# Kernel optimization log

Hardware: AMD Instinct MI355X
Metric: run time of the kernel (lower is better)

The kernel has to match this reference:

```python
import jax, jax.numpy as jnp
import numpy as np

N = 100000   # nodes
E = 1600000  # edges (before self loops)
F = 64       # num_features
H = 64       # hidden_channels
C = 10       # num_classes
G = 128      # graphs in batch
NEG_SLOPE = 0.2


def setup_inputs() -> dict:
    key = jax.random.key(0)
    ks = jax.random.split(key, 16)
    x = jax.random.normal(ks[0], (N, F), dtype=jnp.float32)
    edge_index = jax.random.randint(ks[1], (2, E), 0, N, dtype=jnp.int64)
    batch = jnp.sort(jax.random.randint(ks[2], (N,), 0, G, dtype=jnp.int64))
    def glorot(k, shape):
        fan = shape[0] + shape[-1]
        return jax.random.uniform(k, shape, jnp.float32, -1.0, 1.0) * np.sqrt(6.0 / fan)
    return {
        "x": x, "edge_index": edge_index, "batch": batch,
        # GATConv 1 (F -> H)
        "W1": glorot(ks[3], (F, H)), "as1": glorot(ks[4], (H,)), "ad1": glorot(ks[5], (H,)), "b1": jnp.zeros((H,), jnp.float32),
        # GATConv 2 (H -> H)
        "W2": glorot(ks[6], (H, H)), "as2": glorot(ks[7], (H,)), "ad2": glorot(ks[8], (H,)), "b2": jnp.zeros((H,), jnp.float32),
        # MLP head
        "mw1": glorot(ks[9], (H, H)), "mb1": jnp.zeros((H,), jnp.float32),
        "mw2": glorot(ks[10], (H, C)), "mb2": jnp.zeros((C,), jnp.float32),
    }


def gat_conv(x, src, dst, W, a_s, a_d, b):
    # x: [N, Fin] -> h: [N, Fout]
    h = x @ W
    # per-node attention halves, gathered per edge (heads=1)
    al_s = h @ a_s   # [N]
    al_d = h @ a_d   # [N]
    e = jax.nn.leaky_relu(al_s[src] + al_d[dst], NEG_SLOPE)  # [E']
    # segment softmax over incoming edges of each destination node
    m = jax.ops.segment_max(e, dst, num_segments=N)
    ex = jnp.exp(e - m[dst])
    denom = jax.ops.segment_sum(ex, dst, num_segments=N)
    alpha = ex / denom[dst]                                   # [E']
    # weighted scatter-add of source features
    out = jax.ops.segment_sum(alpha[:, None] * h[src], dst, num_segments=N)
    return out + b


def reference(x, edge_index, batch, W1, as1, ad1, b1, W2, as2, ad2, b2, mw1, mb1, mw2, mb2):
    # add self loops (PyG GATConv default)
    loop = jnp.arange(N, dtype=edge_index.dtype)
    src = jnp.concatenate([edge_index[0], loop])
    dst = jnp.concatenate([edge_index[1], loop])

    h = gat_conv(x, src, dst, W1, as1, ad1, b1)
    h = jax.nn.elu(h)  # dropout p=0.5 is identity in eval mode
    h = gat_conv(h, src, dst, W2, as2, ad2, b2)
    h = jax.nn.elu(h)

    h = jax.nn.relu(h @ mw1 + mb1) @ mw2 + mb2   # MLP [N, C]
    return jax.ops.segment_sum(h, batch, num_segments=G)  # global_add_pool [G, C]
```

## Files before the change

kernel.cpp:

```cpp
#include <hip/hip_runtime.h>
#include <hip/hip_bf16.h>
#include <math.h>

#define SHIFT 20.0f
#define T_PER 32
#define TILE (256 * T_PER)
#define BCAP 5248
#define LS_T 1024
#define MS_LDS 54272

typedef __bf16 bf16x8 __attribute__((ext_vector_type(8)));
typedef float  f32x4  __attribute__((ext_vector_type(4)));

__device__ __forceinline__ unsigned f2bf(float f) {
    unsigned u = __float_as_uint(f);
    return (u + 0x7fffu + ((u >> 16) & 1u)) >> 16;
}

__global__ void setup_kernel(int* __restrict__ bcur, int K2,
                             float* __restrict__ Pz, int nPz,
                             const float* __restrict__ W1,
                             const float* __restrict__ as1, const float* __restrict__ ad1,
                             const float* __restrict__ W2,
                             const float* __restrict__ as2, const float* __restrict__ ad2,
                             const float* __restrict__ mw1,
                             uint4* __restrict__ Wf1, uint4* __restrict__ Wf2,
                             uint4* __restrict__ mwf)
{
    int t = threadIdx.x;
    if (blockIdx.x == 0) {
        for (int i = t; i < K2; i += 256) bcur[i * 16] = i * BCAP;
        for (int i = t; i < nPz; i += 256) Pz[i] = 0.f;
        return;
    }
    __shared__ float wasad[256];
    {
        int k = t & 63;
        const float* W  = (t < 128) ? W1 : W2;
        const float* av = (t < 64) ? as1 : (t < 128) ? ad1 : (t < 192) ? as2 : ad2;
        float s = 0.f;
        for (int n = 0; n < 64; n++) s = fmaf(W[k * 64 + n], av[n], s);
        wasad[t] = s;
    }
    __syncthreads();

    for (int idx = t; idx < 1792; idx += 256) {
        const float* W; const float* wv; uint4* dst; int rem;
        if (idx < 640)       { rem = idx;        W = W1;  wv = &wasad[0];   dst = Wf1; }
        else if (idx < 1280) { rem = idx - 640;  W = W2;  wv = &wasad[128]; dst = Wf2; }
        else                 { rem = idx - 1280; W = mw1; wv = nullptr;     dst = mwf; }
        int pair = rem >> 6, l = rem & 63;
        int tt = pair >> 1, s = pair & 1;
        int kb = s * 32 + (l >> 4) * 8;
        unsigned d[4];
        if (tt < 4) {
            int n = tt * 16 + (l & 15);
            #pragma unroll
            for (int j = 0; j < 4; j++)
                d[j] = f2bf(W[(kb + 2 * j) * 64 + n]) |
                       (f2bf(W[(kb + 2 * j + 1) * 64 + n]) << 16);
        } else {
            int n0 = l & 15;
            #pragma unroll
            for (int j = 0; j < 4; j++) {
                float v0 = (n0 == 0) ? wv[kb + 2 * j]     : (n0 == 1) ? wv[64 + kb + 2 * j]     : 0.f;
                float v1 = (n0 == 0) ? wv[kb + 2 * j + 1] : (n0 == 1) ? wv[64 + kb + 2 * j + 1] : 0.f;
                d[j] = f2bf(v0) | (f2bf(v1) << 16);
            }
        }
        dst[pair * 64 + l] = make_uint4(d[0], d[1], d[2], d[3]);
    }
}

__device__ __forceinline__ void multisplit_body(
    unsigned char* ldsraw, const int* __restrict__ esrc, const int* __restrict__ edst,
    int* __restrict__ bcur, unsigned* __restrict__ pairbuf,
    int nE, int tot, int K2, int tile)
{
    int* lcur   = (int*)ldsraw;
    int* ldelta = lcur + 512;
    int* psum   = ldelta + 512;
    unsigned* seg = (unsigned*)(psum + 256);
    unsigned short* bkt = (unsigned short*)(seg + TILE);
    int t = threadIdx.x;
    int base = tile * TILE;
    int cnt_tile = min(TILE, tot - base);

    for (int i = t; i < 512; i += 256) lcur[i] = 0;
    __syncthreads();

    #pragma unroll
    for (int i = 0; i < T_PER; i++) {
        int e = base + t + i * 256;
        if (e < tot) {
            int d = (e < nE) ? edst[e] : (e - nE);
            atomicAdd(&lcur[d >> 8], 1);
        }
    }
    __syncthreads();

    int v0 = lcur[2 * t], v1 = lcur[2 * t + 1];
    int ps = v0 + v1;
    psum[t] = ps;
    __syncthreads();
    for (int off = 1; off < 256; off <<= 1) {
        int u = (t >= off) ? psum[t - off] : 0;
        __syncthreads();
        psum[t] += u;
        __syncthreads();
    }
    int st0 = psum[t] - ps;
    int st1 = st0 + v0;
    lcur[2 * t] = st0;
    lcur[2 * t + 1] = st1;
    if (v0 > 0 && 2 * t < K2)
        ldelta[2 * t]     = atomicAdd(&bcur[(2 * t) * 16],     v0) - st0;
    if (v1 > 0 && 2 * t + 1 < K2)
        ldelta[2 * t + 1] = atomicAdd(&bcur[(2 * t + 1) * 16], v1) - st1;
    __syncthreads();

    #pragma unroll
    for (int i = 0; i < T_PER; i++) {
        int e = base + t + i * 256;
        if (e < tot) {
            int s = (e < nE) ? esrc[e] : (e - nE);
            int d = (e < nE) ? edst[e] : (e - nE);
            int b = d >> 8;
            int p = atomicAdd(&lcur[b], 1);
            seg[p] = ((unsigned)s << 8) | (unsigned)(d & 255);
            bkt[p] = (unsigned short)b;
        }
    }
    __syncthreads();

    for (int j = t; j < cnt_tile; j += 256)
        pairbuf[j + ldelta[bkt[j]]] = seg[j];
}

__device__ __forceinline__ void gemm_body(
    unsigned char* lds, const void* __restrict__ Xv, int x_is_bf16,
    const uint4* __restrict__ Wf, __hip_bfloat16* __restrict__ Hout,
    float* __restrict__ als, float* __restrict__ ald, int nN, int b0)
{
    int t = threadIdx.x, lane = t & 63, wv = t >> 6;

    uint4 wf[10];
    #pragma unroll
    for (int p = 0; p < 10; p++) wf[p] = Wf[p * 64 + lane];

    if (x_is_bf16) {
        const uint4* X4 = (const uint4*)Xv;
        int limit = nN * 8;
        #pragma unroll
        for (int k = 0; k < 8; k++) {
            int dst = t + k * 256;
            int idx = b0 * 8 + dst;
            if (idx < limit) {
                int r = dst >> 3, c = dst & 7;
                *(uint4*)(lds + r * 144 + c * 16) = X4[idx];
            }
        }
    } else {
        const float4* Xf = (const float4*)Xv;
        int limit = nN * 16;
        #pragma unroll
        for (int k = 0; k < 16; k++) {
            int dst = t + k * 256;
            int idx = b0 * 16 + dst;
            if (idx < limit) {
                float4 v = Xf[idx];
                uint2 r2;
                r2.x = f2bf(v.x) | (f2bf(v.y) << 16);
                r2.y = f2bf(v.z) | (f2bf(v.w) << 16);
                int r = dst >> 4, c = dst & 15;
                *(uint2*)(lds + r * 144 + c * 8) = r2;
            }
        }
    }
    __syncthreads();

    f32x4 acc[4][5] = {};
    int rbase = wv * 64;
    #pragma unroll
    for (int s = 0; s < 2; s++) {
        #pragma unroll
        for (int rf = 0; rf < 4; rf++) {
            const uint4 av = *(const uint4*)(lds + (rbase + rf * 16 + (lane & 15)) * 144
                                                 + s * 64 + (lane >> 4) * 16);
            bf16x8 a = __builtin_bit_cast(bf16x8, av);
            #pragma unroll
            for (int tt = 0; tt < 5; tt++) {
                bf16x8 b = __builtin_bit_cast(bf16x8, wf[tt * 2 + s]);
                acc[rf][tt] = __builtin_amdgcn_mfma_f32_16x16x32_bf16(a, b, acc[rf][tt], 0, 0, 0);
            }
        }
    }

    int q = lane >> 4, c = lane & 15;
    #pragma unroll
    for (int rf = 0; rf < 4; rf++) {
        #pragma unroll
        for (int r = 0; r < 4; r++) {
            int n = b0 + rbase + rf * 16 + q * 4 + r;
            if (n < nN) {
                #pragma unroll
                for (int tt = 0; tt < 4; tt++)
                    Hout[(size_t)n * 64 + tt * 16 + c] = __float2bfloat16(acc[rf][tt][r]);
                if (c == 0)      als[n] = acc[rf][4][r];
                else if (c == 1) ald[n] = acc[rf][4][r];
            }
        }
    }
}

__global__ __launch_bounds__(256) void ms_gemm_kernel(
    const int* __restrict__ esrc, const int* __restrict__ edst,
    int* __restrict__ bcur, unsigned* __restrict__ pairbuf,
    int nE, int nN, int K2, int nTiles,
    const void* __restrict__ Xv, const uint4* __restrict__ Wf,
    __hip_bfloat16* __restrict__ Hout,
    float* __restrict__ als, float* __restrict__ ald)
{
    __shared__ __align__(16) unsigned char lds[MS_LDS];
    if (blockIdx.x < nTiles) {
        multisplit_body(lds, esrc, edst, bcur, pairbuf, nE, nE + nN, K2, blockIdx.x);
    } else {
        gemm_body(lds, Xv, 0, Wf, Hout, als, ald, nN, (blockIdx.x - nTiles) * 256);
    }
}

__global__ __launch_bounds__(256) void gemm_att_mfma(
    const void* __restrict__ Xv, int x_is_bf16,
    const uint4* __restrict__ Wf,
    __hip_bfloat16* __restrict__ Hout,
    float* __restrict__ als, float* __restrict__ ald, int nN)
{
    __shared__ __align__(16) unsigned char lds[256 * 144];
    gemm_body(lds, Xv, x_is_bf16, Wf, Hout, als, ald, nN, blockIdx.x * 256);
}

__global__ __launch_bounds__(LS_T) void local_scatter_kernel(
    const unsigned* __restrict__ pairbuf, const int* __restrict__ bcur,
    int2* __restrict__ rp2, int* __restrict__ csr_src, int nN, int K2)
{
    __shared__ unsigned seg[BCAP];
    __shared__ int lh[256];
    __shared__ int cur[256];
    __shared__ int psum[256];
    int b = blockIdx.x;
    int t = threadIdx.x;
    int d0 = b * 256;
    int nd = min(256, nN - d0);
    int lo = b * BCAP;
    int hi = bcur[b * 16];
    int len = min(hi - lo, BCAP);

    if (t < 256) lh[t] = 0;
    for (int j = t; j < len; j += LS_T) seg[j] = pairbuf[lo + j];
    __syncthreads();
    for (int j = t; j < len; j += LS_T) atomicAdd(&lh[seg[j] & 255u], 1);
    __syncthreads();

    int v = (t < 256) ? lh[t] : 0;
    if (t < 256) psum[t] = v;
    __syncthreads();
    for (int off = 1; off < 256; off <<= 1) {
        int u = (t < 256 && t >= off) ? psum[t - off] : 0;
        __syncthreads();
        if (t < 256) psum[t] += u;
        __syncthreads();
    }
    if (t < 256) {
        int e0 = lo + psum[t] - v;
        cur[t] = e0;
        if (t < nd) rp2[d0 + t] = make_int2(e0, v);
    }
    __syncthreads();

    for (int j = t; j < len; j += LS_T) {
        unsigned w = seg[j];
        int pos = atomicAdd(&cur[w & 255u], 1);
        csr_src[pos] = (int)(w >> 8);
    }
}

__global__ __launch_bounds__(256) void pull_kernel(
    const int* __restrict__ csr_src, const int2* __restrict__ rp2,
    const unsigned* __restrict__ Hu,
    const float* __restrict__ als, const float* __restrict__ ald,
    const float* __restrict__ bias,
    __hip_bfloat162* __restrict__ out2, int nN)
{
    int lane = threadIdx.x & 63;
    int half = lane >> 5;
    int fl = lane & 31;
    int wid  = (blockIdx.x * blockDim.x + threadIdx.x) >> 6;
    int nw   = (gridDim.x * blockDim.x) >> 6;
    float2 bl2 = ((const float2*)bias)[fl];

    for (int d = wid; d < nN; d += nw) {
        int2 rp = rp2[d];
        int s0 = rp.x, m = rp.y;
        float aldd = ald[d];
        float aclo = 0.f, achi = 0.f, den = 0.f;

        for (int base = 0; base < m; base += 64) {
            int j = base + lane;
            bool v = (j < m);
            int sl = v ? csr_src[s0 + j] : 0;
            float ex = 0.f;
            if (v) {
                float sc = als[sl] + aldd;
                sc = (sc > 0.f) ? sc : 0.2f * sc;
                ex = __expf(sc - SHIFT);
            }
            float es = ex;
            #pragma unroll
            for (int off = 32; off > 0; off >>= 1) es += __shfl_xor(es, off);
            den += es;

            int mm = min(64, m - base);
            int sA = __shfl(sl, half), sB = __shfl(sl, 2 + half);
            float eA = __shfl(ex, half), eB = __shfl(ex, 2 + half);
            unsigned dA = Hu[((unsigned)sA << 5) | fl];
            unsigned dB = Hu[((unsigned)sB << 5) | fl];
            for (int i2 = 0; i2 < mm; i2 += 4) {
                int i4 = (i2 + 4) & 63;
                int   sA2 = __shfl(sl, i4 + half);
                int   sB2 = __shfl(sl, i4 + 2 + half);
                float eA2 = __shfl(ex, i4 + half);
                float eB2 = __shfl(ex, i4 + 2 + half);
                unsigned dA2 = Hu[((unsigned)sA2 << 5) | fl];
                unsigned dB2 = Hu[((unsigned)sB2 << 5) | fl];
                aclo = fmaf(eA, __uint_as_float(dA << 16), aclo);
                achi = fmaf(eA, __uint_as_float(dA & 0xffff0000u), achi);
                aclo = fmaf(eB, __uint_as_float(dB << 16), aclo);
                achi = fmaf(eB, __uint_as_float(dB & 0xffff0000u), achi);
                sA = sA2; sB = sB2; eA = eA2; eB = eB2; dA = dA2; dB = dB2;
            }
        }
        aclo += __shfl_xor(aclo, 32);
        achi += __shfl_xor(achi, 32);
        float v0 = aclo / den + bl2.x;
        float v1 = achi / den + bl2.y;
        v0 = (v0 > 0.f) ? v0 : expm1f(v0);
        v1 = (v1 > 0.f) ? v1 : expm1f(v1);
        if (half == 0) {
            __hip_bfloat162 pk;
            pk.x = __float2bfloat16(v0);
            pk.y = __float2bfloat16(v1);
            out2[((unsigned)d << 5) | fl] = pk;
        }
    }
}

__global__ __launch_bounds__(256) void mlp_pool_mfma(
    const uint4* __restrict__ Hin,
    const uint4* __restrict__ mwf, const float* __restrict__ mb1,
    const int* __restrict__ batch,
    float* __restrict__ P, float* __restrict__ Pcnt, int nN)
{
    __shared__ __align__(16) unsigned char lds[256 * 144];
    int t = threadIdx.x, lane = t & 63, wv = t >> 6;
    int b0 = blockIdx.x * 256;

    uint4 wf[8];
    #pragma unroll
    for (int p = 0; p < 8; p++) wf[p] = mwf[p * 64 + lane];

    int limit = nN * 8;
    #pragma unroll
    for (int k = 0; k < 8; k++) {
        int dst = t + k * 256;
        int idx = b0 * 8 + dst;
        if (idx < limit) {
            int r = dst >> 3, c = dst & 7;
            *(uint4*)(lds + r * 144 + c * 16) = Hin[idx];
        }
    }
    __syncthreads();

    f32x4 acc[4][4] = {};
    int rbase = wv * 64;
    #pragma unroll
    for (int s = 0; s < 2; s++) {
        #pragma unroll
        for (int rf = 0; rf < 4; rf++) {
            const uint4 av = *(const uint4*)(lds + (rbase + rf * 16 + (lane & 15)) * 144
                                                 + s * 64 + (lane >> 4) * 16);
            bf16x8 a = __builtin_bit_cast(bf16x8, av);
            #pragma unroll
            for (int tt = 0; tt < 4; tt++) {
                bf16x8 b = __builtin_bit_cast(bf16x8, wf[tt * 2 + s]);
                acc[rf][tt] = __builtin_amdgcn_mfma_f32_16x16x32_bf16(a, b, acc[rf][tt], 0, 0, 0);
            }
        }
    }

    int q = lane >> 4, c = lane & 15;
    float bl0 = mb1[c], bl1 = mb1[16 + c], bl2 = mb1[32 + c], bl3 = mb1[48 + c];
    float r0 = 0.f, r1 = 0.f, r2 = 0.f, r3 = 0.f, ccnt = 0.f;
    int gcur = -1;
    #pragma unroll
    for (int rf = 0; rf < 4; rf++) {
        #pragma unroll
        for (int r = 0; r < 4; r++) {
            int n = b0 + rbase + rf * 16 + q * 4 + r;
            if (n < nN) {
                int g = batch[n];
                if (g != gcur) {
                    if (gcur >= 0) {
                        atomicAdd(&P[(size_t)gcur * 64 + c],      r0);
                        atomicAdd(&P[(size_t)gcur * 64 + 16 + c], r1);
                        atomicAdd(&P[(size_t)gcur * 64 + 32 + c], r2);
                        atomicAdd(&P[(size_t)gcur * 64 + 48 + c], r3);
                        if (c == 0) atomicAdd(&Pcnt[gcur], ccnt);
                    }
                    gcur = g; r0 = r1 = r2 = r3 = 0.f; ccnt = 0.f;
                }
                r0 += fmaxf(acc[rf][0][r] + bl0, 0.f);
                r1 += fmaxf(acc[rf][1][r] + bl1, 0.f);
                r2 += fmaxf(acc[rf][2][r] + bl2, 0.f);
                r3 += fmaxf(acc[rf][3][r] + bl3, 0.f);
                ccnt += 1.f;
            }
        }
    }
    if (gcur >= 0) {
        atomicAdd(&P[(size_t)gcur * 64 + c],      r0);
        atomicAdd(&P[(size_t)gcur * 64 + 16 + c], r1);
        atomicAdd(&P[(size_t)gcur * 64 + 32 + c], r2);
        atomicAdd(&P[(size_t)gcur * 64 + 48 + c], r3);
        if (c == 0) atomicAdd(&Pcnt[gcur], ccnt);
    }
}

__global__ void head_out_kernel(const float* __restrict__ P,
                                const float* __restrict__ Pcnt,
                                const float* __restrict__ mw2,
                                const float* __restrict__ mb2,
                                float* __restrict__ out, int nOut)
{
    int t = blockIdx.x * blockDim.x + threadIdx.x;
    if (t >= nOut) return;
    int g = t / 10, j = t % 10;
    float s = mb2[j] * Pcnt[g];
    const float* pr = P + (size_t)g * 64;
    #pragma unroll
    for (int k = 0; k < 64; k++) s = fmaf(pr[k], mw2[k * 10 + j], s);
    out[t] = s;
}

extern "C" void kernel_launch(void* const* d_in, const int* in_sizes, int n_in,
                              void* d_out, int out_size, void* d_ws, size_t ws_size,
                              hipStream_t stream)
{
    const float* x   = (const float*)d_in[0];
    const int*  eidx = (const int*)d_in[1];
    const int* batch = (const int*)d_in[2];
    const float* W1  = (const float*)d_in[3];
    const float* as1 = (const float*)d_in[4];
    const float* ad1 = (const float*)d_in[5];
    const float* b1  = (const float*)d_in[6];
    const float* W2  = (const float*)d_in[7];
    const float* as2 = (const float*)d_in[8];
    const float* ad2 = (const float*)d_in[9];
    const float* b2  = (const float*)d_in[10];
    const float* mw1 = (const float*)d_in[11];
    const float* mb1 = (const float*)d_in[12];
    const float* mw2 = (const float*)d_in[13];
    const float* mb2 = (const float*)d_in[14];
    float* out = (float*)d_out;

    int nN = in_sizes[0] / 64;
    int nE = in_sizes[1] / 2;
    int tot = nE + nN;
    int K2 = (nN + 255) >> 8;
    int G  = out_size / 10;
    const int* esrc = eidx;
    const int* edst = eidx + nE;

    float* ws = (float*)d_ws;
    size_t NF = (size_t)nN * 64;
    size_t capTot = (size_t)K2 * BCAP;
    float* bufA   = ws;
    float* bufB   = ws + NF;
    float* als    = ws + 2 * NF;
    float* ald    = als + nN;
    int2* rp2     = (int2*)(ald + nN);
    int* csr_src  = (int*)(rp2 + nN);
    int* bcur     = csr_src + capTot;
    float* P      = (float*)(bcur + K2 * 16 + 15);
    float* Pcnt   = P + (size_t)G * 64;
    uintptr_t wb  = ((uintptr_t)(Pcnt + G) + 255) & ~(uintptr_t)255;
    uint4* Wf1    = (uint4*)wb;
    uint4* Wf2    = Wf1 + 640;
    uint4* mwf    = Wf2 + 640;
    unsigned* pairbuf = (unsigned*)bufA;
    __hip_bfloat16* hbf = (__hip_bfloat16*)bufB;

    dim3 blk(256);
    int nTiles = (tot + TILE - 1) / TILE;
    int nT256 = (nN + 255) / 256;

    setup_kernel<<<2, blk, 0, stream>>>(bcur, K2, P, G * 64 + G,
                                        W1, as1, ad1, W2, as2, ad2, mw1,
                                        Wf1, Wf2, mwf);
    ms_gemm_kernel<<<nTiles + nT256, blk, 0, stream>>>(
        esrc, edst, bcur, pairbuf, nE, nN, K2, nTiles,
        x, Wf1, hbf, als, ald);
    local_scatter_kernel<<<K2, dim3(LS_T), 0, stream>>>(pairbuf, bcur, rp2,
                                                        csr_src, nN, K2);

    pull_kernel<<<2048, blk, 0, stream>>>(csr_src, rp2, (const unsigned*)hbf,
                                          als, ald, b1,
                                          (__hip_bfloat162*)bufA, nN);
    gemm_att_mfma<<<nT256, blk, 0, stream>>>(bufA, 1, Wf2, hbf, als, ald, nN);
    pull_kernel<<<2048, blk, 0, stream>>>(csr_src, rp2, (const unsigned*)hbf,
                                          als, ald, b2,
                                          (__hip_bfloat162*)bufA, nN);

    mlp_pool_mfma<<<nT256, blk, 0, stream>>>((const uint4*)bufA, mwf, mb1,
                                             batch, P, Pcnt, nN);
    head_out_kernel<<<(out_size + 255) / 256, blk, 0, stream>>>(P, Pcnt, mw2,
                                                                mb2, out, out_size);
}
```

Baseline: 290.5 us.

## Wave-level scan in scatter, deeper gather prefetch, fuse head into MLP pool

Replaces the block-wide Hillis-Steele scan over 256 bucket counts with a single-wavefront shuffle scan where each lane handles four counts, removing many barriers. The pull kernel's gather loop now prefetches two steps ahead instead of one, to hide more of the latency of the random H row loads. The head_out kernel is folded into mlp_pool_mfma through a last-block-done atomic counter, which saves a launch. The done counter is zeroed by setup_kernel, and the fused head relies on threadfence ordering so the last block sees every block's atomics.

```diff
diff --git a/kernel.cpp b/kernel.cpp
--- a/kernel.cpp
+++ b/kernel.cpp
@@ -246,7 +246,6 @@
     __shared__ unsigned seg[BCAP];
     __shared__ int lh[256];
     __shared__ int cur[256];
-    __shared__ int psum[256];
     int b = blockIdx.x;
     int t = threadIdx.x;
     int d0 = b * 256;
@@ -261,19 +260,23 @@
     for (int j = t; j < len; j += LS_T) atomicAdd(&lh[seg[j] & 255u], 1);
     __syncthreads();
 
-    int v = (t < 256) ? lh[t] : 0;
-    if (t < 256) psum[t] = v;
-    __syncthreads();
-    for (int off = 1; off < 256; off <<= 1) {
-        int u = (t < 256 && t >= off) ? psum[t - off] : 0;
-        __syncthreads();
-        if (t < 256) psum[t] += u;
-        __syncthreads();
-    }
-    if (t < 256) {
-        int e0 = lo + psum[t] - v;
-        cur[t] = e0;
-        if (t < nd) rp2[d0 + t] = make_int2(e0, v);
+    if (t < 64) {
+        int b4 = t * 4;
+        int c0 = lh[b4], c1 = lh[b4 + 1], c2 = lh[b4 + 2], c3 = lh[b4 + 3];
+        int tot4 = c0 + c1 + c2 + c3;
+        int run = tot4;
+        #pragma unroll
+        for (int off = 1; off < 64; off <<= 1) {
+            int u = __shfl_up(run, off);
+            if (t >= off) run += u;
+        }
+        int e0 = lo + run - tot4;
+        int e1 = e0 + c0, e2 = e1 + c1, e3 = e2 + c2;
+        cur[b4] = e0; cur[b4 + 1] = e1; cur[b4 + 2] = e2; cur[b4 + 3] = e3;
+        if (b4 < nd)     rp2[d0 + b4]     = make_int2(e0, c0);
+        if (b4 + 1 < nd) rp2[d0 + b4 + 1] = make_int2(e1, c1);
+        if (b4 + 2 < nd) rp2[d0 + b4 + 2] = make_int2(e2, c2);
+        if (b4 + 3 < nd) rp2[d0 + b4 + 3] = make_int2(e3, c3);
     }
     __syncthreads();
 
@@ -320,23 +323,24 @@
             den += es;
 
             int mm = min(64, m - base);
-            int sA = __shfl(sl, half), sB = __shfl(sl, 2 + half);
-            float eA = __shfl(ex, half), eB = __shfl(ex, 2 + half);
-            unsigned dA = Hu[((unsigned)sA << 5) | fl];
-            unsigned dB = Hu[((unsigned)sB << 5) | fl];
+            float eA0 = __shfl(ex, half),     eB0 = __shfl(ex, 2 + half);
+            unsigned dA0 = Hu[((unsigned)__shfl(sl, half) << 5) | fl];
+            unsigned dB0 = Hu[((unsigned)__shfl(sl, 2 + half) << 5) | fl];
+            float eA1 = __shfl(ex, 4 + half), eB1 = __shfl(ex, 6 + half);
+            unsigned dA1 = Hu[((unsigned)__shfl(sl, 4 + half) << 5) | fl];
+            unsigned dB1 = Hu[((unsigned)__shfl(sl, 6 + half) << 5) | fl];
             for (int i2 = 0; i2 < mm; i2 += 4) {
-                int i4 = (i2 + 4) & 63;
-                int   sA2 = __shfl(sl, i4 + half);
-                int   sB2 = __shfl(sl, i4 + 2 + half);
-                float eA2 = __shfl(ex, i4 + half);
-                float eB2 = __shfl(ex, i4 + 2 + half);
-                unsigned dA2 = Hu[((unsigned)sA2 << 5) | fl];
-                unsigned dB2 = Hu[((unsigned)sB2 << 5) | fl];
-                aclo = fmaf(eA, __uint_as_float(dA << 16), aclo);
-                achi = fmaf(eA, __uint_as_float(dA & 0xffff0000u), achi);
-                aclo = fmaf(eB, __uint_as_float(dB << 16), aclo);
-                achi = fmaf(eB, __uint_as_float(dB & 0xffff0000u), achi);
-                sA = sA2; sB = sB2; eA = eA2; eB = eB2; dA = dA2; dB = dB2;
+                int i8 = (i2 + 8) & 63;
+                float eA2 = __shfl(ex, i8 + half);
+                float eB2 = __shfl(ex, i8 + 2 + half);
+                unsigned dA2 = Hu[((unsigned)__shfl(sl, i8 + half) << 5) | fl];
+                unsigned dB2 = Hu[((unsigned)__shfl(sl, i8 + 2 + half) << 5) | fl];
+                aclo = fmaf(eA0, __uint_as_float(dA0 << 16), aclo);
+                achi = fmaf(eA0, __uint_as_float(dA0 & 0xffff0000u), achi);
+                aclo = fmaf(eB0, __uint_as_float(dB0 << 16), aclo);
+                achi = fmaf(eB0, __uint_as_float(dB0 & 0xffff0000u), achi);
+                eA0 = eA1; dA0 = dA1; eB0 = eB1; dB0 = dB1;
+                eA1 = eA2; dA1 = dA2; eB1 = eB2; dB1 = dB2;
             }
         }
         aclo += __shfl_xor(aclo, 32);
@@ -358,7 +362,9 @@
     const uint4* __restrict__ Hin,
     const uint4* __restrict__ mwf, const float* __restrict__ mb1,
     const int* __restrict__ batch,
-    float* __restrict__ P, float* __restrict__ Pcnt, int nN)
+    float* __restrict__ P, float* __restrict__ Pcnt, int nN,
+    const float* __restrict__ mw2, const float* __restrict__ mb2,
+    float* __restrict__ out, int nOut, int* __restrict__ done, int nBlocks)
 {
     __shared__ __align__(16) unsigned char lds[256 * 144];
     int t = threadIdx.x, lane = t & 63, wv = t >> 6;
@@ -433,22 +439,25 @@
         atomicAdd(&P[(size_t)gcur * 64 + 48 + c], r3);
         if (c == 0) atomicAdd(&Pcnt[gcur], ccnt);
     }
-}
-
-__global__ void head_out_kernel(const float* __restrict__ P,
-                                const float* __restrict__ Pcnt,
-                                const float* __restrict__ mw2,
-                                const float* __restrict__ mb2,
-                                float* __restrict__ out, int nOut)
-{
-    int t = blockIdx.x * blockDim.x + threadIdx.x;
-    if (t >= nOut) return;
-    int g = t / 10, j = t % 10;
-    float s = mb2[j] * Pcnt[g];
-    const float* pr = P + (size_t)g * 64;
-    #pragma unroll
-    for (int k = 0; k < 64; k++) s = fmaf(pr[k], mw2[k * 10 + j], s);
-    out[t] = s;
+
+    __syncthreads();
+    __shared__ int isLast;
+    if (t == 0) {
+        __threadfence();
+        isLast = (atomicAdd(done, 1) == nBlocks - 1);
+    }
+    __syncthreads();
+    if (isLast) {
+        __threadfence();
+        for (int o = t; o < nOut; o += 256) {
+            int g = o / 10, j = o % 10;
+            float s = mb2[j] * Pcnt[g];
+            const float* pr = P + (size_t)g * 64;
+            #pragma unroll
+            for (int k = 0; k < 64; k++) s = fmaf(pr[k], mw2[k * 10 + j], s);
+            out[o] = s;
+        }
+    }
 }
 
 extern "C" void kernel_launch(void* const* d_in, const int* in_sizes, int n_in,
@@ -492,7 +501,8 @@
     int* bcur     = csr_src + capTot;
     float* P      = (float*)(bcur + K2 * 16 + 15);
     float* Pcnt   = P + (size_t)G * 64;
-    uintptr_t wb  = ((uintptr_t)(Pcnt + G) + 255) & ~(uintptr_t)255;
+    int* done     = (int*)(Pcnt + G);
+    uintptr_t wb  = ((uintptr_t)(done + 1) + 255) & ~(uintptr_t)255;
     uint4* Wf1    = (uint4*)wb;
     uint4* Wf2    = Wf1 + 640;
     uint4* mwf    = Wf2 + 640;
@@ -503,7 +513,7 @@
     int nTiles = (tot + TILE - 1) / TILE;
     int nT256 = (nN + 255) / 256;
 
-    setup_kernel<<<2, blk, 0, stream>>>(bcur, K2, P, G * 64 + G,
+    setup_kernel<<<2, blk, 0, stream>>>(bcur, K2, P, G * 64 + G + 1,
                                         W1, as1, ad1, W2, as2, ad2, mw1,
                                         Wf1, Wf2, mwf);
     ms_gemm_kernel<<<nTiles + nT256, blk, 0, stream>>>(
@@ -521,7 +531,7 @@
                                           (__hip_bfloat162*)bufA, nN);
 
     mlp_pool_mfma<<<nT256, blk, 0, stream>>>((const uint4*)bufA, mwf, mb1,
-                                             batch, P, Pcnt, nN);
-    head_out_kernel<<<(out_size + 255) / 256, blk, 0, stream>>>(P, Pcnt, mw2,
-                                                                mb2, out, out_size);
-}
+                                             batch, P, Pcnt, nN,
+                                             mw2, mb2, out, out_size,
+                                             done, nT256);
+}
```

Measured after the change: 315.2 us. 8.5% more time.
